# Performance work log

Measured on AMD Instinct MI355X. Metric: run time of the kernel, lower is better.

The kernel has to match this reference:

```python
import jax, jax.numpy as jnp
import numpy as np
import math

B, S, E, H, FF = 8, 1024, 1024, 16, 4096
HD = E // H
N_DOM = 1024          # boolean-domain size used in the custom scale
LN_EPS = 1e-5


def _layernorm(x, g, b, eps=LN_EPS):
    mu = jnp.mean(x, axis=-1, keepdims=True)
    var = jnp.var(x, axis=-1, keepdims=True)
    return (x - mu) * jax.lax.rsqrt(var + eps) * g + b


def setup_inputs() -> dict:
    key = jax.random.key(0)
    ks = jax.random.split(key, 8)
    s_e = 1.0 / math.sqrt(E)
    s_f = 1.0 / math.sqrt(FF)
    return {
        "x": jax.random.normal(ks[0], (B, S, E), jnp.float32),
        "in_proj_w": jax.random.normal(ks[1], (3 * E, E), jnp.float32) * s_e,
        "out_proj_w": jax.random.normal(ks[2], (E, E), jnp.float32) * s_e,
        "ln1_g": jnp.ones((E,), jnp.float32),
        "ln1_b": jnp.zeros((E,), jnp.float32),
        "ln2_g": jnp.ones((E,), jnp.float32),
        "ln2_b": jnp.zeros((E,), jnp.float32),
        "w1": jax.random.normal(ks[3], (FF, E), jnp.float32) * s_e,
        "b1": jax.random.normal(ks[4], (FF,), jnp.float32) * 0.01,
        "w2": jax.random.normal(ks[5], (E, FF), jnp.float32) * s_f,
        "b2": jax.random.normal(ks[6], (E,), jnp.float32) * 0.01,
    }


def reference(x, in_proj_w, out_proj_w, ln1_g, ln1_b, ln2_g, ln2_b, w1, b1, w2, b2):
    # --- custom multi-head attention (bias=False, dropout=0) ---
    qkv = jnp.einsum("bse,fe->bsf", x, in_proj_w)              # [B,S,3E]
    q, k, v = jnp.split(qkv, 3, axis=-1)
    q = q.reshape(B, S, H, HD)
    k = k.reshape(B, S, H, HD)
    v = v.reshape(B, S, H, HD)
    # nonstandard scale: sqrt(1/head_dim) * 2 * log(N)
    scale = math.sqrt(1.0 / HD) * 2.0 * math.log(N_DOM)
    scores = jnp.einsum("bqhd,bkhd->bhqk", q * scale, k)       # [B,H,S,S]
    attn = jax.nn.softmax(scores, axis=-1)
    ctx = jnp.einsum("bhqk,bkhd->bqhd", attn, v).reshape(B, S, E)
    attn_out = jnp.einsum("bse,fe->bsf", ctx, out_proj_w)      # [B,S,E]
    # --- residual + norm + FFN + residual + norm ---
    h = _layernorm(x + attn_out, ln1_g, ln1_b)
    ff = jnp.einsum("bsf,ef->bse", jax.nn.relu(jnp.einsum("bse,fe->bsf", h, w1) + b1), w2) + b2
    return _layernorm(h + ff, ln2_g, ln2_b)
```

## Files before the change

kernel.cpp:

```cpp
#include <hip/hip_runtime.h>
#include <cstdint>
#include <cmath>


typedef _Float16 f16;
typedef _Float16 f16x8 __attribute__((ext_vector_type(8)));
typedef _Float16 f16x4 __attribute__((ext_vector_type(4)));
typedef __bf16   bf16;
typedef __bf16   bf16x8 __attribute__((ext_vector_type(8)));
typedef __bf16   bf16x4 __attribute__((ext_vector_type(4)));
typedef __bf16   bf16x2 __attribute__((ext_vector_type(2)));
typedef float    f32x4  __attribute__((ext_vector_type(4)));
typedef float    f32x16 __attribute__((ext_vector_type(16)));
typedef unsigned int uint2v __attribute__((ext_vector_type(2)));
typedef unsigned int u32x4v __attribute__((ext_vector_type(4)));

#define B_SZ  8
#define S_SZ  1024
#define E_SZ  1024
#define H_SZ  16
#define HD_SZ 64
#define FF_SZ 4096
#define MTOK  (B_SZ * S_SZ)

__device__ __forceinline__ void async_ld16(const void* g, void* l) {
  __builtin_amdgcn_global_load_lds(
      (const __attribute__((address_space(1))) void*)(uintptr_t)g,
      (__attribute__((address_space(3))) void*)(uint32_t)(uintptr_t)l,
      16, 0, 0);
}

template <int N>
__device__ __forceinline__ void wait_vm() {
  if constexpr (N == 0)      asm volatile("s_waitcnt vmcnt(0)" ::: "memory");
  else if constexpr (N == 3) asm volatile("s_waitcnt vmcnt(3)" ::: "memory");
  else if constexpr (N == 4) asm volatile("s_waitcnt vmcnt(4)" ::: "memory");
  else static_assert(N == 0 || N == 3 || N == 4, "unsupported vmcnt");
  __builtin_amdgcn_sched_barrier(0);
}

__device__ __forceinline__ void wait_lgkm0_fenced() {
  asm volatile("s_waitcnt lgkmcnt(0)" ::: "memory");
  __builtin_amdgcn_sched_barrier(0);
}

__device__ __forceinline__ void permswap(uint32_t& a, uint32_t& b) {
  uint2v r = __builtin_amdgcn_permlane32_swap(a, b, false, false);
  a = r[0];
  b = r[1];
}

__global__ void cast_all_kernel(const float* __restrict__ wqkv, const float* __restrict__ wo,
                                const float* __restrict__ w1, const float* __restrict__ w2,
                                const float* __restrict__ x,
                                f16* __restrict__ w_inb, f16* __restrict__ w_outb,
                                f16* __restrict__ w1b, f16* __restrict__ w2b,
                                f16* __restrict__ xb) {
  const int i = blockIdx.x * blockDim.x + threadIdx.x;
  const float* src;
  f16* dst;
  int off;
  if (i < 786432)       { src = wqkv; dst = w_inb;  off = i; }
  else if (i < 1048576) { src = wo;   dst = w_outb; off = i - 786432; }
  else if (i < 2097152) { src = w1;   dst = w1b;    off = i - 1048576; }
  else if (i < 3145728) { src = w2;   dst = w2b;    off = i - 2097152; }
  else                  { src = x;    dst = xb;     off = i - 3145728; }
  float4 f = ((const float4*)src)[off];
  f16x4 o = {(f16)f.x, (f16)f.y, (f16)f.z, (f16)f.w};
  ((f16x4*)dst)[off] = o;
}

template <int BN, bool OUT_F16, bool RELU>
__global__ __launch_bounds__(512, 2)
void gemm256(const f16* __restrict__ A, const f16* __restrict__ Bm,
             const float* __restrict__ bias, void* __restrict__ Cp,
             int M, int N, int K, int bf16_from_col) {
  static_assert(BN == 256 || BN == 128, "BN must be 256 or 128");
  static_assert(!(OUT_F16 && BN == 128), "f16 LDS epilogue requires BN==256");
  constexpr int NBCH  = (BN == 256) ? 2 : 1;
  constexpr int CHUNK = 4096;
  constexpr int NIF   = 2 + NBCH;
  constexpr int WN    = (BN == 256) ? 4 : 2;
  constexpr int FM    = (BN == 256) ? 8 : 4;

  __shared__ f16 lds[(8 + 4 * NBCH) * CHUNK];
  f16* Ab = lds;
  f16* Bb = lds + 8 * CHUNK;

  const int tid  = threadIdx.x;
  const int wave = tid >> 6;
  const int lane = tid & 63;
  const int quad = lane >> 4;
  const int l16  = lane & 15;

  const int wm  = wave / WN;
  const int wn  = wave % WN;
  const int ah  = (BN == 256) ? wm : (wm >> 1);
  const int amB = (BN == 256) ? 0 : (wm & 1) * 64;
  const int bh  = (BN == 256) ? (wn >> 1) : 0;
  const int bnB = (BN == 256) ? (wn & 1) * 64 : wn * 64;

  const int gx = N / BN;
  int bm, bn;
  {
    const int b   = blockIdx.x;
    const int nwg = gridDim.x;
    const int gm  = nwg / gx;
    if (((nwg & 63) == 0) && ((gx & 1) == 0) && ((gm & 3) == 0)) {
      const int xcd = b & 7;
      const int seq = b >> 3;
      const int st  = xcd + ((seq >> 3) << 3);
      const int pos = seq & 7;
      const int nstx = gx >> 1;
      bn = (st % nstx) * 2 + (pos & 1);
      bm = (st / nstx) * 4 + (pos >> 1);
    } else {
      int logical = b;
      if ((nwg & 7) == 0) logical = (logical & 7) * (nwg >> 3) + (logical >> 3);
      bn = logical % gx;
      bm = logical / gx;
    }
  }

  f32x4 acc[FM][4];
#pragma unroll
  for (int mi = 0; mi < FM; mi++)
#pragma unroll
    for (int ni = 0; ni < 4; ni++) acc[mi][ni] = (f32x4){0.f, 0.f, 0.f, 0.f};

  const int rr_s = tid >> 2;
  const int lo_s = (tid & 3) ^ ((rr_s >> 1) & 3);
  const int wofs = wave * 512;
  const f16* gAb = A  + ((size_t)bm * 256 + rr_s) * (size_t)K + lo_s * 8;
  const f16* gBb = Bm + ((size_t)bn * BN  + rr_s) * (size_t)K + lo_s * 8;

  auto stA = [&](int bb, int s, int h, int kt) {
    async_ld16(gAb + (size_t)h * 128 * K + kt * 64 + s * 32,
               Ab + ((((bb << 1) + s) << 1) + h) * CHUNK + wofs);
  };
  auto stB = [&](int bb, int s, int h, int kt) {
    async_ld16(gBb + (size_t)h * 128 * K + kt * 64 + s * 32,
               Bb + (((bb << 1) + s) * NBCH + h) * CHUNK + wofs);
  };
  auto rdFrag = [&](const f16* ch, int rr) -> f16x8 {
    return *(const f16x8*)&ch[rr * 32 + ((quad ^ ((rr >> 1) & 3)) << 3)];
  };

  const int NT = K >> 6;

#pragma unroll
  for (int s = 0; s < 2; s++) {
    stA(0, s, 0, 0);
    stA(0, s, 1, 0);
    stB(0, s, 0, 0);
    if constexpr (NBCH == 2) stB(0, s, 1, 0);
  }
  wait_vm<NIF>();
  __builtin_amdgcn_s_barrier();

  for (int t = 0; t < NT; t++) {
    const int cur = t & 1, oth = cur ^ 1;
    const bool last = (t == NT - 1);
#pragma unroll
    for (int s = 0; s < 2; s++) {
      const f16* Ach = Ab + ((((cur << 1) + s) << 1) + ah) * CHUNK;
      const f16* Bch = Bb + (((cur << 1) + s) * NBCH + bh) * CHUNK;

      f16x8 bfr[4], af[4];
#pragma unroll
      for (int ni = 0; ni < 4; ni++) bfr[ni] = rdFrag(Bch, bnB + ni * 16 + l16);
#pragma unroll
      for (int i = 0; i < 4; i++) af[i] = rdFrag(Ach, amB + i * 16 + l16);
      if (!last) {
        stA(oth, s, 0, t + 1);
        stA(oth, s, 1, t + 1);
        if constexpr (NBCH == 1) stB(oth, s, 0, t + 1);
      }
      __builtin_amdgcn_sched_barrier(0);
      __builtin_amdgcn_s_barrier();
      wait_lgkm0_fenced();
      __builtin_amdgcn_s_setprio(1);
#pragma unroll
      for (int i = 0; i < 4; i++)
#pragma unroll
        for (int ni = 0; ni < 4; ni++)
          acc[i][ni] = __builtin_amdgcn_mfma_f32_16x16x32_f16(bfr[ni], af[i], acc[i][ni], 0, 0, 0);
      __builtin_amdgcn_s_setprio(0);

      if constexpr (BN == 256) {
        __builtin_amdgcn_s_barrier();
#pragma unroll
        for (int i = 0; i < 4; i++) af[i] = rdFrag(Ach, amB + (4 + i) * 16 + l16);
        if (!last) {
          stB(oth, s, 0, t + 1);
          stB(oth, s, 1, t + 1);
        }
        __builtin_amdgcn_sched_barrier(0);
        __builtin_amdgcn_s_barrier();
        wait_lgkm0_fenced();
        __builtin_amdgcn_s_setprio(1);
#pragma unroll
        for (int i = 0; i < 4; i++)
#pragma unroll
          for (int ni = 0; ni < 4; ni++)
            acc[4 + i][ni] = __builtin_amdgcn_mfma_f32_16x16x32_f16(bfr[ni], af[i], acc[4 + i][ni], 0, 0, 0);
        __builtin_amdgcn_s_setprio(0);
      }

      if (!last) {
        wait_vm<NIF>();
        __builtin_amdgcn_s_barrier();
      } else if (s == 0) {
        wait_vm<0>();
        __builtin_amdgcn_s_barrier();
      }
    }
  }

  if constexpr (!OUT_F16) {
    const int rowG0 = bm * 256 + ((BN == 256) ? wm * 128 : wm * 64);
    const int colG0 = bn * BN + wn * 64;
    float* Cf = (float*)Cp;
#pragma unroll
    for (int ni = 0; ni < 4; ni++) {
      const int col = colG0 + ni * 16 + quad * 4;
      float4 bv = {0.f, 0.f, 0.f, 0.f};
      if (bias != nullptr) bv = *(const float4*)&bias[col];
#pragma unroll
      for (int mi = 0; mi < FM; mi++) {
        const int row = rowG0 + mi * 16 + l16;
        float v0 = acc[mi][ni][0] + bv.x;
        float v1 = acc[mi][ni][1] + bv.y;
        float v2 = acc[mi][ni][2] + bv.z;
        float v3 = acc[mi][ni][3] + bv.w;
        if (RELU) {
          v0 = fmaxf(v0, 0.f); v1 = fmaxf(v1, 0.f);
          v2 = fmaxf(v2, 0.f); v3 = fmaxf(v3, 0.f);
        }
        f32x4 o = {v0, v1, v2, v3};
        *(f32x4*)&Cf[(size_t)row * N + col] = o;
      }
    }
  } else {
    __syncthreads();
    {
      char* cb = (char*)lds;
      const int rowL0 = wm * 128;
      const int colL0 = wn * 64;
      const bool store_bf16 = (bn * BN >= bf16_from_col);
#pragma unroll
      for (int mi = 0; mi < FM; mi++) {
        const int row = rowL0 + mi * 16 + l16;
        const int sw  = row & 7;
#pragma unroll
        for (int ni = 0; ni < 4; ni++) {
          const int col = colL0 + ni * 16 + quad * 4;
          float4 bv = {0.f, 0.f, 0.f, 0.f};
          if (bias != nullptr) bv = *(const float4*)&bias[bn * BN + col];
          float v0 = acc[mi][ni][0] + bv.x;
          float v1 = acc[mi][ni][1] + bv.y;
          float v2 = acc[mi][ni][2] + bv.z;
          float v3 = acc[mi][ni][3] + bv.w;
          if (RELU) {
            v0 = fmaxf(v0, 0.f); v1 = fmaxf(v1, 0.f);
            v2 = fmaxf(v2, 0.f); v3 = fmaxf(v3, 0.f);
          }
          const int ch = (col >> 3) ^ sw;
          char* p = cb + row * 512 + (ch << 4) + ((quad & 1) << 3);
          if (store_bf16) {
            bf16x4 o = {(bf16)v0, (bf16)v1, (bf16)v2, (bf16)v3};
            *(bf16x4*)p = o;
          } else {
            f16x4 o = {(f16)v0, (f16)v1, (f16)v2, (f16)v3};
            *(f16x4*)p = o;
          }
        }
      }
    }
    __syncthreads();
    {
      const char* cb = (const char*)lds;
      const int rr0 = tid >> 5;
      const int cc  = tid & 31;
      const size_t rowBytes = (size_t)N * 2;
      char* gbase = (char*)Cp + (size_t)(bm * 256) * rowBytes
                  + (size_t)bn * BN * 2 + (size_t)cc * 16;
#pragma unroll
      for (int it = 0; it < 16; it++) {
        const int row = it * 16 + rr0;
        const int ch  = cc ^ (row & 7);
        u32x4v v = *(const u32x4v*)(cb + row * 512 + (ch << 4));
        *(u32x4v*)(gbase + (size_t)row * rowBytes) = v;
      }
    }
  }
  (void)M;
}

__global__ __launch_bounds__(256, 4)
void attn_kernel(const f16* __restrict__ qkv, f16* __restrict__ ctx,
                 float scale2, float c2) {
  __shared__ __align__(16) char pool[33280];
  f16*  Ks = (f16*)pool;
  bf16* Vt = (bf16*)(pool + 16384);

  const int tid  = threadIdx.x;
  const int wave = tid >> 6;
  const int lane = tid & 63;
  const int l31  = lane & 31;
  const int hi   = lane >> 5;

  const int flat = blockIdx.x;
  const int bh   = flat & 127;
  const int qt   = flat >> 7;
  const int b    = bh >> 4;
  const int h    = bh & 15;

  const int rs = 3 * E_SZ;
  const size_t tokbase = (size_t)b * S_SZ;

  const int su  = lane >> 3;
  const int soc = (lane & 7) ^ su;

  {
    const f16* gq = qkv + (tokbase + qt * 128 + wave * 8 + su) * (size_t)rs + h * HD_SZ + soc * 8;
#pragma unroll
    for (int i = 0; i < 4; i++)
      async_ld16(gq + (size_t)i * 32 * rs, pool + (i * 32 + wave * 8) * 128);
  }
  __syncthreads();

  f16x8 aq[4];
  {
    const int qrow = wave * 32 + l31;
#pragma unroll
    for (int ks = 0; ks < 4; ks++)
      aq[ks] = *(const f16x8*)&Ks[qrow * 64 + (((ks * 2 + hi) ^ (qrow & 7)) << 3)];
  }

  float Lp = 0.f;
  f32x16 oacc[2];
#pragma unroll
  for (int nb = 0; nb < 2; nb++)
#pragma unroll
    for (int i = 0; i < 16; i++) oacc[nb][i] = 0.f;

  const int vc  = (tid & 7) * 8;
  const int vk0 = (tid >> 3) * 4;

  for (int t = 0; t < S_SZ / 128; t++) {
    __syncthreads();
    {
      const f16* gk = qkv + (tokbase + t * 128 + wave * 8 + su) * (size_t)rs + E_SZ + h * HD_SZ + soc * 8;
#pragma unroll
      for (int i = 0; i < 4; i++)
        async_ld16(gk + (size_t)i * 32 * rs, pool + (i * 32 + wave * 8) * 128);
    }
    {
      const bf16* gv = (const bf16*)qkv + (tokbase + t * 128 + vk0) * (size_t)rs + 2 * E_SZ + h * HD_SZ + vc;
      bf16x8 v0 = *(const bf16x8*)(gv);
      bf16x8 v1 = *(const bf16x8*)(gv + rs);
      bf16x8 v2 = *(const bf16x8*)(gv + 2 * rs);
      bf16x8 v3 = *(const bf16x8*)(gv + 3 * rs);
#pragma unroll
      for (int e = 0; e < 8; e++) {
        bf16x4 pk = {v0[e], v1[e], v2[e], v3[e]};
        *(bf16x4*)&Vt[(vc + e) * 132 + vk0] = pk;
      }
    }
    __syncthreads();

#pragma unroll
    for (int nt = 0; nt < 4; nt++) {
      f32x16 sacc;
#pragma unroll
      for (int i = 0; i < 16; i++) sacc[i] = 0.f;

      const int krow = nt * 32 + l31;
      __builtin_amdgcn_s_setprio(1);
#pragma unroll
      for (int ks = 0; ks < 4; ks++) {
        f16x8 kf = *(const f16x8*)&Ks[krow * 64 + (((ks * 2 + hi) ^ (krow & 7)) << 3)];
        sacc = __builtin_amdgcn_mfma_f32_32x32x16_f16(kf, aq[ks], sacc, 0, 0, 0);
      }
      __builtin_amdgcn_s_setprio(0);

      uint32_t w[8];
#pragma unroll
      for (int j = 0; j < 8; j++) {
        float p0 = exp2f(fmaf(sacc[2 * j],     scale2, -c2));
        float p1 = exp2f(fmaf(sacc[2 * j + 1], scale2, -c2));
        Lp += p0 + p1;
        bf16x2 pk2 = {(bf16)p0, (bf16)p1};
        w[j] = __builtin_bit_cast(uint32_t, pk2);
      }
      permswap(w[0], w[2]);
      permswap(w[1], w[3]);
      permswap(w[4], w[6]);
      permswap(w[5], w[7]);
      u32x4v pe = {w[0], w[1], w[2], w[3]};
      u32x4v po = {w[4], w[5], w[6], w[7]};
      bf16x8 pa[2] = {__builtin_bit_cast(bf16x8, pe), __builtin_bit_cast(bf16x8, po)};

      __builtin_amdgcn_s_setprio(1);
#pragma unroll
      for (int nb = 0; nb < 2; nb++) {
        const int d = nb * 32 + l31;
#pragma unroll
        for (int kst = 0; kst < 2; kst++) {
          const int key = (nt * 2 + kst) * 16 + hi * 8;
          bf16x4 blo = *(const bf16x4*)&Vt[d * 132 + key];
          bf16x4 bhi = *(const bf16x4*)&Vt[d * 132 + key + 4];
          bf16x8 bv = __builtin_shufflevector(blo, bhi, 0, 1, 2, 3, 4, 5, 6, 7);
          oacc[nb] = __builtin_amdgcn_mfma_f32_32x32x16_bf16(pa[kst], bv, oacc[nb], 0, 0, 0);
        }
      }
      __builtin_amdgcn_s_setprio(0);
    }
  }

  float Lfull = Lp + __shfl_xor(Lp, 32, 64);
  const float inv = 1.f / Lfull;
#pragma unroll
  for (int r = 0; r < 16; r++) {
    const int qrow = (r & 3) + 8 * (r >> 2) + 4 * hi;
    const float invr = __shfl(inv, qrow, 32);
    const size_t row = tokbase + (size_t)qt * 128 + wave * 32 + qrow;
#pragma unroll
    for (int nb = 0; nb < 2; nb++)
      ctx[row * (size_t)E_SZ + h * HD_SZ + nb * 32 + l31] = (f16)(oacc[nb][r] * invr);
  }
}

__global__ void ln_kernel(const float* __restrict__ a, const float* __restrict__ res,
                          const float* __restrict__ g, const float* __restrict__ bta,
                          float* __restrict__ out32, f16* __restrict__ out16) {
  const int row  = blockIdx.x;
  const int tid  = threadIdx.x;
  const int wave = tid >> 6;
  const int lane = tid & 63;
  const size_t base = (size_t)row * 1024;
  const int c = tid * 4;

  float4 va = *(const float4*)&a[base + c];
  float4 vr = *(const float4*)&res[base + c];
  float v0 = va.x + vr.x, v1 = va.y + vr.y, v2 = va.z + vr.z, v3 = va.w + vr.w;

  __shared__ float r1[4], r2[4];
  float s = v0 + v1 + v2 + v3;
#pragma unroll
  for (int off = 32; off; off >>= 1) s += __shfl_xor(s, off, 64);
  if (lane == 0) r1[wave] = s;
  __syncthreads();
  const float mu = (r1[0] + r1[1] + r1[2] + r1[3]) * (1.f / 1024.f);

  float d0 = v0 - mu, d1 = v1 - mu, d2 = v2 - mu, d3 = v3 - mu;
  float ss = d0 * d0 + d1 * d1 + d2 * d2 + d3 * d3;
#pragma unroll
  for (int off = 32; off; off >>= 1) ss += __shfl_xor(ss, off, 64);
  if (lane == 0) r2[wave] = ss;
  __syncthreads();
  const float var = (r2[0] + r2[1] + r2[2] + r2[3]) * (1.f / 1024.f);
  const float rsq = rsqrtf(var + 1e-5f);

  float4 gg = *(const float4*)&g[c];
  float4 bb = *(const float4*)&bta[c];
  float o0 = d0 * rsq * gg.x + bb.x;
  float o1 = d1 * rsq * gg.y + bb.y;
  float o2 = d2 * rsq * gg.z + bb.z;
  float o3 = d3 * rsq * gg.w + bb.w;
  float4 o = {o0, o1, o2, o3};
  *(float4*)&out32[base + c] = o;
  if (out16 != nullptr) {
    f16x4 ob = {(f16)o0, (f16)o1, (f16)o2, (f16)o3};
    *(f16x4*)&out16[base + c] = ob;
  }
}

extern "C" void kernel_launch(void* const* d_in, const int* in_sizes, int n_in,
                              void* d_out, int out_size, void* d_ws, size_t ws_size,
                              hipStream_t stream) {
  const float* x    = (const float*)d_in[0];
  const float* wqkv = (const float*)d_in[1];
  const float* wo   = (const float*)d_in[2];
  const float* ln1g = (const float*)d_in[3];
  const float* ln1b = (const float*)d_in[4];
  const float* ln2g = (const float*)d_in[5];
  const float* ln2b = (const float*)d_in[6];
  const float* w1   = (const float*)d_in[7];
  const float* b1   = (const float*)d_in[8];
  const float* w2   = (const float*)d_in[9];
  const float* b2   = (const float*)d_in[10];
  float* out = (float*)d_out;

  char* ws = (char*)d_ws;
  f16* w_inb  = (f16*)(ws + 0);
  f16* w_outb = (f16*)(ws + 6291456);
  f16* w1b    = (f16*)(ws + 8388608);
  f16* w2b    = (f16*)(ws + 16777216);
  f16* xb     = (f16*)(ws + 25165824);
  f16* qkv    = (f16*)(ws + 41943040);
  f16* ctx    = (f16*)(ws + 92274688);
  f16* ff1    = (f16*)(ws + 41943040);
  float* tmp  = (float*)(ws + 109051904);
  float* hbuf = (float*)(ws + 142606336);
  f16* hb     = xb;

  const int NOBF = 1 << 30;

  cast_all_kernel<<<20480, 256, 0, stream>>>(wqkv, wo, w1, w2, x,
                                             w_inb, w_outb, w1b, w2b, xb);

  gemm256<256, true, false><<<(3 * E_SZ / 256) * (MTOK / 256), 512, 0, stream>>>(
      xb, w_inb, nullptr, qkv, MTOK, 3 * E_SZ, E_SZ, 2048);

  attn_kernel<<<1024, 256, 0, stream>>>(qkv, ctx, 2.5f, 60.0f);

  gemm256<128, false, false><<<(E_SZ / 128) * (MTOK / 256), 512, 0, stream>>>(
      ctx, w_outb, nullptr, tmp, MTOK, E_SZ, E_SZ, NOBF);

  ln_kernel<<<MTOK, 256, 0, stream>>>(tmp, x, ln1g, ln1b, hbuf, hb);

  gemm256<256, true, true><<<(FF_SZ / 256) * (MTOK / 256), 512, 0, stream>>>(
      hb, w1b, b1, ff1, MTOK, FF_SZ, E_SZ, NOBF);

  gemm256<128, false, false><<<(E_SZ / 128) * (MTOK / 256), 512, 0, stream>>>(
      ff1, w2b, b2, tmp, MTOK, E_SZ, FF_SZ, NOBF);

  ln_kernel<<<MTOK, 256, 0, stream>>>(tmp, hbuf, ln2g, ln2b, out, nullptr);

  (void)in_sizes; (void)n_in; (void)out_size; (void)ws_size;
}
```

Measured before the change: 481.9 us.

## Double-buffer K tiles, prefetch V into registers, fold scale and row-sum into MFMA

The attention kernel now double-buffers K tiles in LDS and prefetches the next V tile into registers, so global loads overlap the current tile's MFMA work. The softmax scale is folded into Q once, and the -c2 offset seeds the score accumulator, which removes a per-element FMA. Row sums are computed with an extra MFMA against a ones vector instead of scalar adds plus shuffles. The larger LDS footprint lowers the occupancy hint from 4 to 3 blocks per CU, and rounding Q*scale to f16 and summing bf16-rounded probabilities changes numerics slightly.

```diff
diff --git a/kernel.cpp b/kernel.cpp
--- a/kernel.cpp
+++ b/kernel.cpp
@@ -297,12 +297,11 @@
   (void)M;
 }
 
-__global__ __launch_bounds__(256, 4)
+__global__ __launch_bounds__(256, 3)
 void attn_kernel(const f16* __restrict__ qkv, f16* __restrict__ ctx,
                  float scale2, float c2) {
-  __shared__ __align__(16) char pool[33280];
-  f16*  Ks = (f16*)pool;
-  bf16* Vt = (bf16*)(pool + 16384);
+  __shared__ __align__(16) char pool[49664];
+  bf16* Vt = (bf16*)(pool + 32768);
 
   const int tid  = threadIdx.x;
   const int wave = tid >> 6;
@@ -332,55 +331,85 @@
 
   f16x8 aq[4];
   {
+    const f16* Q0 = (const f16*)pool;
     const int qrow = wave * 32 + l31;
-#pragma unroll
-    for (int ks = 0; ks < 4; ks++)
-      aq[ks] = *(const f16x8*)&Ks[qrow * 64 + (((ks * 2 + hi) ^ (qrow & 7)) << 3)];
-  }
-
-  float Lp = 0.f;
-  f32x16 oacc[2];
-#pragma unroll
-  for (int nb = 0; nb < 2; nb++)
-#pragma unroll
-    for (int i = 0; i < 16; i++) oacc[nb][i] = 0.f;
+    const f16 sc = (f16)scale2;
+    const f16x8 sc8 = {sc, sc, sc, sc, sc, sc, sc, sc};
+#pragma unroll
+    for (int ks = 0; ks < 4; ks++) {
+      f16x8 q = *(const f16x8*)&Q0[qrow * 64 + (((ks * 2 + hi) ^ (qrow & 7)) << 3)];
+      aq[ks] = q * sc8;
+    }
+  }
+  __syncthreads();
 
   const int vc  = (tid & 7) * 8;
   const int vk0 = (tid >> 3) * 4;
+
+  {
+    const f16* gk = qkv + (tokbase + 0 * 128 + wave * 8 + su) * (size_t)rs + E_SZ + h * HD_SZ + soc * 8;
+#pragma unroll
+    for (int i = 0; i < 4; i++)
+      async_ld16(gk + (size_t)i * 32 * rs, pool + (i * 32 + wave * 8) * 128);
+  }
+  bf16x8 vr0, vr1, vr2, vr3;
+  {
+    const bf16* gv = (const bf16*)qkv + (tokbase + 0 * 128 + vk0) * (size_t)rs + 2 * E_SZ + h * HD_SZ + vc;
+    vr0 = *(const bf16x8*)(gv);
+    vr1 = *(const bf16x8*)(gv + rs);
+    vr2 = *(const bf16x8*)(gv + 2 * rs);
+    vr3 = *(const bf16x8*)(gv + 3 * rs);
+  }
+
+  f32x16 oacc[2];
+  f32x16 Lacc;
+#pragma unroll
+  for (int nb = 0; nb < 2; nb++)
+#pragma unroll
+    for (int i = 0; i < 16; i++) oacc[nb][i] = 0.f;
+#pragma unroll
+  for (int i = 0; i < 16; i++) Lacc[i] = 0.f;
+
+  const bf16 one = (bf16)1.0f;
+  const bf16x8 onesb = {one, one, one, one, one, one, one, one};
+  const float negc2 = -c2;
 
   for (int t = 0; t < S_SZ / 128; t++) {
     __syncthreads();
     {
-      const f16* gk = qkv + (tokbase + t * 128 + wave * 8 + su) * (size_t)rs + E_SZ + h * HD_SZ + soc * 8;
+#pragma unroll
+      for (int e = 0; e < 8; e++) {
+        bf16x4 pk = {vr0[e], vr1[e], vr2[e], vr3[e]};
+        *(bf16x4*)&Vt[(vc + e) * 132 + vk0] = pk;
+      }
+    }
+    __syncthreads();
+
+    if (t < S_SZ / 128 - 1) {
+      const f16* gk = qkv + (tokbase + (t + 1) * 128 + wave * 8 + su) * (size_t)rs + E_SZ + h * HD_SZ + soc * 8;
 #pragma unroll
       for (int i = 0; i < 4; i++)
-        async_ld16(gk + (size_t)i * 32 * rs, pool + (i * 32 + wave * 8) * 128);
-    }
-    {
-      const bf16* gv = (const bf16*)qkv + (tokbase + t * 128 + vk0) * (size_t)rs + 2 * E_SZ + h * HD_SZ + vc;
-      bf16x8 v0 = *(const bf16x8*)(gv);
-      bf16x8 v1 = *(const bf16x8*)(gv + rs);
-      bf16x8 v2 = *(const bf16x8*)(gv + 2 * rs);
-      bf16x8 v3 = *(const bf16x8*)(gv + 3 * rs);
-#pragma unroll
-      for (int e = 0; e < 8; e++) {
-        bf16x4 pk = {v0[e], v1[e], v2[e], v3[e]};
-        *(bf16x4*)&Vt[(vc + e) * 132 + vk0] = pk;
-      }
-    }
-    __syncthreads();
+        async_ld16(gk + (size_t)i * 32 * rs, pool + ((t + 1) & 1) * 16384 + (i * 32 + wave * 8) * 128);
+      const bf16* gv = (const bf16*)qkv + (tokbase + (t + 1) * 128 + vk0) * (size_t)rs + 2 * E_SZ + h * HD_SZ + vc;
+      vr0 = *(const bf16x8*)(gv);
+      vr1 = *(const bf16x8*)(gv + rs);
+      vr2 = *(const bf16x8*)(gv + 2 * rs);
+      vr3 = *(const bf16x8*)(gv + 3 * rs);
+    }
+
+    const f16* Kcur = (const f16*)(pool + (t & 1) * 16384);
 
 #pragma unroll
     for (int nt = 0; nt < 4; nt++) {
       f32x16 sacc;
 #pragma unroll
-      for (int i = 0; i < 16; i++) sacc[i] = 0.f;
+      for (int i = 0; i < 16; i++) sacc[i] = negc2;
 
       const int krow = nt * 32 + l31;
       __builtin_amdgcn_s_setprio(1);
 #pragma unroll
       for (int ks = 0; ks < 4; ks++) {
-        f16x8 kf = *(const f16x8*)&Ks[krow * 64 + (((ks * 2 + hi) ^ (krow & 7)) << 3)];
+        f16x8 kf = *(const f16x8*)&Kcur[krow * 64 + (((ks * 2 + hi) ^ (krow & 7)) << 3)];
         sacc = __builtin_amdgcn_mfma_f32_32x32x16_f16(kf, aq[ks], sacc, 0, 0, 0);
       }
       __builtin_amdgcn_s_setprio(0);
@@ -388,9 +417,8 @@
       uint32_t w[8];
 #pragma unroll
       for (int j = 0; j < 8; j++) {
-        float p0 = exp2f(fmaf(sacc[2 * j],     scale2, -c2));
-        float p1 = exp2f(fmaf(sacc[2 * j + 1], scale2, -c2));
-        Lp += p0 + p1;
+        float p0 = exp2f(sacc[2 * j]);
+        float p1 = exp2f(sacc[2 * j + 1]);
         bf16x2 pk2 = {(bf16)p0, (bf16)p1};
         w[j] = __builtin_bit_cast(uint32_t, pk2);
       }
@@ -403,6 +431,8 @@
       bf16x8 pa[2] = {__builtin_bit_cast(bf16x8, pe), __builtin_bit_cast(bf16x8, po)};
 
       __builtin_amdgcn_s_setprio(1);
+      Lacc = __builtin_amdgcn_mfma_f32_32x32x16_bf16(pa[0], onesb, Lacc, 0, 0, 0);
+      Lacc = __builtin_amdgcn_mfma_f32_32x32x16_bf16(pa[1], onesb, Lacc, 0, 0, 0);
 #pragma unroll
       for (int nb = 0; nb < 2; nb++) {
         const int d = nb * 32 + l31;
@@ -419,12 +449,10 @@
     }
   }
 
-  float Lfull = Lp + __shfl_xor(Lp, 32, 64);
-  const float inv = 1.f / Lfull;
 #pragma unroll
   for (int r = 0; r < 16; r++) {
+    const float invr = 1.f / Lacc[r];
     const int qrow = (r & 3) + 8 * (r >> 2) + 4 * hi;
-    const float invr = __shfl(inv, qrow, 32);
     const size_t row = tokbase + (size_t)qt * 128 + wave * 32 + qrow;
 #pragma unroll
     for (int nb = 0; nb < 2; nb++)
```

After: 489.3 us. Within noise of the previous version (+1.5%).
